# Optimization experiments

Measured on AMD Instinct MI355X. Metric: run time of the kernel, lower is better.

The kernel has to match this reference:

```python
import jax, jax.numpy as jnp
import numpy as np

B, S, D = 2, 2048, 1024
H, DK, DV = 16, 64, 64
NEG = -1e9

def setup_inputs() -> dict:
    key = jax.random.key(0)
    ks = jax.random.split(key, 7)
    scale = 1.0 / np.sqrt(D)
    return {
        "Q": jax.random.normal(ks[0], (B, S, D), dtype=jnp.float32),
        "K": jax.random.normal(ks[1], (B, S, D), dtype=jnp.float32),
        "V": jax.random.normal(ks[2], (B, S, D), dtype=jnp.float32),
        "Wq": jax.random.normal(ks[3], (D, H * DK), dtype=jnp.float32) * scale,
        "Wk": jax.random.normal(ks[4], (D, H * DK), dtype=jnp.float32) * scale,
        "Wv": jax.random.normal(ks[5], (D, H * DV), dtype=jnp.float32) * scale,
        "Wo": jax.random.normal(ks[6], (H * DV, D), dtype=jnp.float32) * scale,
    }

def reference(Q, K, V, Wq, Wk, Wv, Wo):
    b, sq, _ = Q.shape
    sk = K.shape[1]
    # project and split heads: [b, h, s, d]
    q = (Q @ Wq).reshape(b, sq, H, DK).transpose(0, 2, 1, 3)
    k = (K @ Wk).reshape(b, sk, H, DK).transpose(0, 2, 1, 3)
    v = (V @ Wv).reshape(b, sk, H, DV).transpose(0, 2, 1, 3)
    scores = jnp.einsum("bhqd,bhkd->bhqk", q, k) / jnp.sqrt(jnp.float32(DK))
    causal = jnp.tril(jnp.ones((sq, sk), dtype=bool))
    scores = jnp.where(causal[None, None], scores, NEG)
    attn = jax.nn.softmax(scores, axis=-1)
    out = jnp.einsum("bhqk,bhkd->bhqd", attn, v)
    out = out.transpose(0, 2, 1, 3).reshape(b, sq, H * DV)
    return out @ Wo
```

## Files before the change

kernel.cpp:

```cpp
#include <hip/hip_runtime.h>
#include <cstdint>
#include <cstddef>


typedef __bf16 bf16x8 __attribute__((ext_vector_type(8)));
typedef __bf16 bf16x4 __attribute__((ext_vector_type(4)));
typedef float f32x4 __attribute__((ext_vector_type(4)));
typedef unsigned int u32x4 __attribute__((ext_vector_type(4)));

#define MFMA __builtin_amdgcn_mfma_f32_16x16x32_bf16

static __device__ __forceinline__ __bf16 f2b(float f) { return (__bf16)f; }

static __device__ __forceinline__ void gload_lds16(const void* g, void* l) {
  __builtin_amdgcn_global_load_lds(
      (const __attribute__((address_space(1))) void*)g,
      (__attribute__((address_space(3))) void*)l, 16, 0, 0);
}

__global__ __launch_bounds__(256) void wtrans_kernel(
    const float* __restrict__ w0, const float* __restrict__ w1,
    const float* __restrict__ w2, const float* __restrict__ w3,
    __bf16* __restrict__ outT)
{
  const int z = blockIdx.z;
  const float* W = (z == 0) ? w0 : (z == 1) ? w1 : (z == 2) ? w2 : w3;
  __bf16* O = outT + (size_t)z * 1048576;
  __shared__ float t[32][33];
  const int tx = threadIdx.x & 31, ty = threadIdx.x >> 5;
  const int kb = blockIdx.y * 32, nb = blockIdx.x * 32;
#pragma unroll
  for (int i = 0; i < 4; i++)
    t[ty + i * 8][tx] = W[(size_t)(kb + ty + i * 8) * 1024 + nb + tx];
  __syncthreads();
#pragma unroll
  for (int i = 0; i < 4; i++)
    O[(size_t)(nb + ty + i * 8) * 1024 + kb + tx] = f2b(t[tx][ty + i * 8]);
}

__global__ __launch_bounds__(256) void cvt_kernel(
    const float* __restrict__ a0, const float* __restrict__ a1,
    const float* __restrict__ a2, __bf16* __restrict__ o0,
    __bf16* __restrict__ o1, __bf16* __restrict__ o2)
{
  const int z = blockIdx.y;
  const float* src = (z == 0) ? a0 : (z == 1) ? a1 : a2;
  __bf16* dst = (z == 0) ? o0 : (z == 1) ? o1 : o2;
  const int idx = blockIdx.x * 256 + threadIdx.x;
#pragma unroll
  for (int it = 0; it < 4; ++it) {
    const size_t c = (size_t)(idx + it * 131072) * 8;
    f32x4 v0 = *(const f32x4*)&src[c];
    f32x4 v1 = *(const f32x4*)&src[c + 4];
    bf16x8 w = {f2b(v0[0]), f2b(v0[1]), f2b(v0[2]), f2b(v0[3]),
                f2b(v1[0]), f2b(v1[1]), f2b(v1[2]), f2b(v1[3])};
    *(bf16x8*)&dst[c] = w;
  }
}

__global__ __launch_bounds__(256) void gemm_proj_bf16_kernel(
    const __bf16* __restrict__ A0, const __bf16* __restrict__ A1,
    const __bf16* __restrict__ A2, const __bf16* __restrict__ WT,
    __bf16* __restrict__ C0, __bf16* __restrict__ C1, __bf16* __restrict__ C2)
{
  const int z = blockIdx.y;
  const __bf16* A = (z == 0) ? A0 : (z == 1) ? A1 : A2;
  const __bf16* W = WT + (size_t)z * 1048576;
  __bf16* C = (z == 0) ? C0 : (z == 1) ? C1 : C2;

  const int bid = blockIdx.x;
  const int t = (bid & 7) * 32 + (bid >> 3);
  const int mt = t >> 3, nt = t & 7;
  const int mbase = mt * 128, nbase = nt * 128;

  __shared__ __align__(16) __bf16 As[128][32];
  __shared__ __align__(16) __bf16 Bs[128][32];

  const int tid = threadIdx.x;
  const int wid = tid >> 6, lane = tid & 63;
  const int wr = wid >> 1, wc = wid & 1;
  const int lr = lane & 15, kg = lane >> 4;

  f32x4 acc[4][4] = {};

  const int srow = tid >> 2, scol = (tid & 3) * 8;
  const int wbase = tid & 192;

  for (int kb = 0; kb < 32; ++kb) {
    const int k0 = kb * 32;
    __syncthreads();
#pragma unroll
    for (int p = 0; p < 2; ++p) {
      const int r = srow + p * 64;
      gload_lds16(&A[(size_t)(mbase + r) * 1024 + k0 + scol],
                  (__bf16*)As + (size_t)(p * 256 + wbase) * 8);
      gload_lds16(&W[(size_t)(nbase + r) * 1024 + k0 + scol],
                  (__bf16*)Bs + (size_t)(p * 256 + wbase) * 8);
    }
    __syncthreads();

    bf16x8 af[4], bfr[4];
#pragma unroll
    for (int i = 0; i < 4; i++) af[i] = *(const bf16x8*)&As[wr * 64 + i * 16 + lr][kg * 8];
#pragma unroll
    for (int j = 0; j < 4; j++) bfr[j] = *(const bf16x8*)&Bs[wc * 64 + j * 16 + lr][kg * 8];
#pragma unroll
    for (int i = 0; i < 4; i++)
#pragma unroll
      for (int j = 0; j < 4; j++)
        acc[i][j] = MFMA(af[i], bfr[j], acc[i][j], 0, 0, 0);
  }

  if (z == 2) {
#pragma unroll
    for (int i = 0; i < 4; i++)
#pragma unroll
      for (int j = 0; j < 4; j++) {
        const int m0 = mbase + wr * 64 + i * 16 + kg * 4;
        const int n = nbase + wc * 64 + j * 16 + lr;
        const int b = m0 >> 11, s = m0 & 2047, h = n >> 6, dv = n & 63;
        bf16x4 w;
#pragma unroll
        for (int r = 0; r < 4; r++) w[r] = f2b(acc[i][j][r]);
        *(bf16x4*)&C[(((size_t)(b * 16 + h)) * 64 + dv) * 2048 + s] = w;
      }
  } else {
#pragma unroll
    for (int i = 0; i < 4; i++)
#pragma unroll
      for (int j = 0; j < 4; j++)
#pragma unroll
        for (int r = 0; r < 4; r++) {
          const int m = mbase + wr * 64 + i * 16 + kg * 4 + r;
          const int n = nbase + wc * 64 + j * 16 + lr;
          const int b = m >> 11, s = m & 2047, h = n >> 6, dk = n & 63;
          C[(((size_t)(b * 16 + h)) * 2048 + s) * 64 + dk] = f2b(acc[i][j][r]);
        }
  }
}

__global__ __launch_bounds__(256) void gemm_proj_f32_kernel(
    const float* __restrict__ A0, const float* __restrict__ A1,
    const float* __restrict__ A2, const __bf16* __restrict__ WT,
    __bf16* __restrict__ C0, __bf16* __restrict__ C1, __bf16* __restrict__ C2)
{
  const int z = blockIdx.y;
  const float* A = (z == 0) ? A0 : (z == 1) ? A1 : A2;
  const __bf16* W = WT + (size_t)z * 1048576;
  __bf16* C = (z == 0) ? C0 : (z == 1) ? C1 : C2;

  const int mt = blockIdx.x >> 3, nt = blockIdx.x & 7;
  const int mbase = mt * 128, nbase = nt * 128;

  __shared__ __align__(16) __bf16 As[128][40];
  __shared__ __align__(16) __bf16 Bs[128][40];

  const int tid = threadIdx.x;
  const int wid = tid >> 6, lane = tid & 63;
  const int wr = wid >> 1, wc = wid & 1;
  const int lr = lane & 15, kg = lane >> 4;

  f32x4 acc[4][4] = {};
  const int arow = tid >> 3, ac0 = (tid & 7) * 4;

  for (int kb = 0; kb < 32; ++kb) {
    const int k0 = kb * 32;
#pragma unroll
    for (int p = 0; p < 4; ++p) {
      const int r = arow + p * 32;
      f32x4 av = *(const f32x4*)&A[(size_t)(mbase + r) * 1024 + k0 + ac0];
      bf16x4 cv = {f2b(av[0]), f2b(av[1]), f2b(av[2]), f2b(av[3])};
      *(bf16x4*)&As[r][ac0] = cv;
    }
#pragma unroll
    for (int p = 0; p < 2; ++p) {
      const int idx = p * 256 + tid;
      const int r = idx >> 2, c8 = (idx & 3) * 8;
      *(u32x4*)&Bs[r][c8] = *(const u32x4*)&W[(size_t)(nbase + r) * 1024 + k0 + c8];
    }
    __syncthreads();

    bf16x8 af[4], bfr[4];
#pragma unroll
    for (int i = 0; i < 4; i++) af[i] = *(const bf16x8*)&As[wr * 64 + i * 16 + lr][kg * 8];
#pragma unroll
    for (int j = 0; j < 4; j++) bfr[j] = *(const bf16x8*)&Bs[wc * 64 + j * 16 + lr][kg * 8];
#pragma unroll
    for (int i = 0; i < 4; i++)
#pragma unroll
      for (int j = 0; j < 4; j++)
        acc[i][j] = MFMA(af[i], bfr[j], acc[i][j], 0, 0, 0);
    __syncthreads();
  }

  if (z == 2) {
#pragma unroll
    for (int i = 0; i < 4; i++)
#pragma unroll
      for (int j = 0; j < 4; j++) {
        const int m0 = mbase + wr * 64 + i * 16 + kg * 4;
        const int n = nbase + wc * 64 + j * 16 + lr;
        const int b = m0 >> 11, s = m0 & 2047, h = n >> 6, dv = n & 63;
        bf16x4 w;
#pragma unroll
        for (int r = 0; r < 4; r++) w[r] = f2b(acc[i][j][r]);
        *(bf16x4*)&C[(((size_t)(b * 16 + h)) * 64 + dv) * 2048 + s] = w;
      }
  } else {
#pragma unroll
    for (int i = 0; i < 4; i++)
#pragma unroll
      for (int j = 0; j < 4; j++)
#pragma unroll
        for (int r = 0; r < 4; r++) {
          const int m = mbase + wr * 64 + i * 16 + kg * 4 + r;
          const int n = nbase + wc * 64 + j * 16 + lr;
          const int b = m >> 11, s = m & 2047, h = n >> 6, dk = n & 63;
          C[(((size_t)(b * 16 + h)) * 2048 + s) * 64 + dk] = f2b(acc[i][j][r]);
        }
  }
}

__global__ __launch_bounds__(256) void attn_kernel(
    const __bf16* __restrict__ Qh, const __bf16* __restrict__ Kh,
    const __bf16* __restrict__ VTh, __bf16* __restrict__ AO)
{
  const int lin = blockIdx.y * 16 + blockIdx.x;
  const int l = (lin & 7) * 64 + (lin >> 3);
  const int xp = l & 15, bh = l >> 4;
  const int b = bh >> 4, h = bh & 15;
  const __bf16* Qp = Qh + (size_t)bh * 2048 * 64;
  const __bf16* Kp = Kh + (size_t)bh * 2048 * 64;
  const __bf16* Vp = VTh + (size_t)bh * 64 * 2048;

  __shared__ __align__(16) __bf16 Ks[2][64][72];
  __shared__ __align__(16) __bf16 Vt[2][64][72];
  __shared__ __align__(16) __bf16 Ps[4][16][72];

  const int tid = threadIdx.x, wid = tid >> 6, lane = tid & 63;
  const int lr = lane & 15, kg = lane >> 4;
  const int sr0 = tid >> 3, sc0 = (tid & 7) * 8;
  const float SCALE = 0.125f * 1.44269504f;

#pragma unroll
  for (int phase = 0; phase < 2; ++phase) {
    const int qblk = phase ? (31 - xp) : xp;
    const int qbase = qblk << 6;
    const int nkv = qblk + 1;
    const int wq = qbase + wid * 16;

    bf16x8 qf0 = *(const bf16x8*)&Qp[(size_t)(wq + lr) * 64 + kg * 8];
    bf16x8 qf1 = *(const bf16x8*)&Qp[(size_t)(wq + lr) * 64 + 32 + kg * 8];

    f32x4 ot[4] = {};
    float mrow = -1e30f, lsum = 0.f;

    u32x4 kr0 = *(const u32x4*)&Kp[(size_t)sr0 * 64 + sc0];
    u32x4 kr1 = *(const u32x4*)&Kp[(size_t)(sr0 + 32) * 64 + sc0];
    u32x4 vr0 = *(const u32x4*)&Vp[(size_t)sr0 * 2048 + sc0];
    u32x4 vr1 = *(const u32x4*)&Vp[(size_t)(sr0 + 32) * 2048 + sc0];
    __syncthreads();
    *(u32x4*)&Ks[0][sr0][sc0] = kr0;
    *(u32x4*)&Ks[0][sr0 + 32][sc0] = kr1;
    *(u32x4*)&Vt[0][sr0][sc0] = vr0;
    *(u32x4*)&Vt[0][sr0 + 32][sc0] = vr1;

    int cur = 0;
    for (int t = 0; t < nkv; ++t) {
      const int kv0 = t << 6;
      const bool pre = (t + 1 < nkv);
      if (pre) {
        const int nkv0 = kv0 + 64;
        kr0 = *(const u32x4*)&Kp[(size_t)(nkv0 + sr0) * 64 + sc0];
        kr1 = *(const u32x4*)&Kp[(size_t)(nkv0 + sr0 + 32) * 64 + sc0];
        vr0 = *(const u32x4*)&Vp[(size_t)sr0 * 2048 + nkv0 + sc0];
        vr1 = *(const u32x4*)&Vp[(size_t)(sr0 + 32) * 2048 + nkv0 + sc0];
      }
      __syncthreads();

      if (kv0 <= wq + 15) {
        f32x4 st[4] = {};
        __builtin_amdgcn_s_setprio(1);
#pragma unroll
        for (int kvt = 0; kvt < 4; ++kvt) {
          bf16x8 kf0 = *(const bf16x8*)&Ks[cur][kvt * 16 + lr][kg * 8];
          bf16x8 kf1 = *(const bf16x8*)&Ks[cur][kvt * 16 + lr][32 + kg * 8];
          st[kvt] = MFMA(kf0, qf0, st[kvt], 0, 0, 0);
          st[kvt] = MFMA(kf1, qf1, st[kvt], 0, 0, 0);
        }
        __builtin_amdgcn_s_setprio(0);

        const int qidx = wq + lr;
        const bool needmask = (kv0 + 63) > wq;
        float sv[16];
        float mx = -1e30f;
#pragma unroll
        for (int kvt = 0; kvt < 4; ++kvt)
#pragma unroll
          for (int r = 0; r < 4; ++r) {
            float v = st[kvt][r] * SCALE;
            if (needmask && (kv0 + kvt * 16 + kg * 4 + r > qidx)) v = -1e30f;
            sv[kvt * 4 + r] = v;
            mx = fmaxf(mx, v);
          }
        mx = fmaxf(mx, __shfl_xor(mx, 16));
        mx = fmaxf(mx, __shfl_xor(mx, 32));
        const float mnew = fmaxf(mrow, mx);
        const float scl = exp2f(mrow - mnew);
        mrow = mnew;
        float rs = 0.f;
#pragma unroll
        for (int kvt = 0; kvt < 4; ++kvt) {
          bf16x4 pk;
#pragma unroll
          for (int r = 0; r < 4; ++r) {
            const float p = exp2f(sv[kvt * 4 + r] - mnew);
            rs += p;
            pk[r] = f2b(p);
          }
          *(bf16x4*)&Ps[wid][lr][kvt * 16 + kg * 4] = pk;
        }
        rs += __shfl_xor(rs, 16);
        rs += __shfl_xor(rs, 32);
        lsum = lsum * scl + rs;
#pragma unroll
        for (int dvt = 0; dvt < 4; ++dvt) ot[dvt] *= scl;

#pragma unroll
        for (int h2 = 0; h2 < 2; ++h2) {
          bf16x8 pf = *(const bf16x8*)&Ps[wid][lr][h2 * 32 + kg * 8];
          __builtin_amdgcn_s_setprio(1);
#pragma unroll
          for (int dvt = 0; dvt < 4; ++dvt) {
            bf16x8 vf = *(const bf16x8*)&Vt[cur][dvt * 16 + lr][h2 * 32 + kg * 8];
            ot[dvt] = MFMA(vf, pf, ot[dvt], 0, 0, 0);
          }
          __builtin_amdgcn_s_setprio(0);
        }
      }

      if (pre) {
        const int nb = cur ^ 1;
        *(u32x4*)&Ks[nb][sr0][sc0] = kr0;
        *(u32x4*)&Ks[nb][sr0 + 32][sc0] = kr1;
        *(u32x4*)&Vt[nb][sr0][sc0] = vr0;
        *(u32x4*)&Vt[nb][sr0 + 32][sc0] = vr1;
      }
      cur ^= 1;
    }

    const float rl = 1.f / lsum;
    const int q = wq + lr;
#pragma unroll
    for (int dvt = 0; dvt < 4; ++dvt) {
      bf16x4 w;
#pragma unroll
      for (int r = 0; r < 4; ++r) w[r] = f2b(ot[dvt][r] * rl);
      *(bf16x4*)&AO[((size_t)(b * 2048 + q)) * 1024 + h * 64 + dvt * 16 + kg * 4] = w;
    }
  }
}

__global__ __launch_bounds__(256) void gemm_out_kernel(
    const __bf16* __restrict__ A, const __bf16* __restrict__ WT,
    float* __restrict__ Out)
{
  const int bid = blockIdx.x;
  const int t = (bid & 7) * 32 + (bid >> 3);
  const int mt = t >> 3, nt = t & 7;
  const int mbase = mt * 128, nbase = nt * 128;

  __shared__ __align__(16) __bf16 As[128][32];
  __shared__ __align__(16) __bf16 Bs[128][32];

  const int tid = threadIdx.x;
  const int wid = tid >> 6, lane = tid & 63;
  const int wr = wid >> 1, wc = wid & 1;
  const int lr = lane & 15, kg = lane >> 4;

  f32x4 acc[4][4] = {};

  const int srow = tid >> 2, scol = (tid & 3) * 8;
  const int wbase = tid & 192;

  for (int kb = 0; kb < 32; ++kb) {
    const int k0 = kb * 32;
    __syncthreads();
#pragma unroll
    for (int p = 0; p < 2; ++p) {
      const int r = srow + p * 64;
      gload_lds16(&A[(size_t)(mbase + r) * 1024 + k0 + scol],
                  (__bf16*)As + (size_t)(p * 256 + wbase) * 8);
      gload_lds16(&WT[(size_t)(nbase + r) * 1024 + k0 + scol],
                  (__bf16*)Bs + (size_t)(p * 256 + wbase) * 8);
    }
    __syncthreads();

    bf16x8 af[4], bfr[4];
#pragma unroll
    for (int i = 0; i < 4; i++) af[i] = *(const bf16x8*)&As[wr * 64 + i * 16 + lr][kg * 8];
#pragma unroll
    for (int j = 0; j < 4; j++) bfr[j] = *(const bf16x8*)&Bs[wc * 64 + j * 16 + lr][kg * 8];
#pragma unroll
    for (int i = 0; i < 4; i++)
#pragma unroll
      for (int j = 0; j < 4; j++)
        acc[i][j] = MFMA(af[i], bfr[j], acc[i][j], 0, 0, 0);
  }

#pragma unroll
  for (int i = 0; i < 4; i++)
#pragma unroll
    for (int j = 0; j < 4; j++)
#pragma unroll
      for (int r = 0; r < 4; r++) {
        const int m = mbase + wr * 64 + i * 16 + kg * 4 + r;
        const int n = nbase + wc * 64 + j * 16 + lr;
        Out[(size_t)m * 1024 + n] = acc[i][j][r];
      }
}

extern "C" void kernel_launch(void* const* d_in, const int* in_sizes, int n_in,
                              void* d_out, int out_size, void* d_ws, size_t ws_size,
                              hipStream_t stream) {
  const float* Q  = (const float*)d_in[0];
  const float* K  = (const float*)d_in[1];
  const float* V  = (const float*)d_in[2];
  const float* Wq = (const float*)d_in[3];
  const float* Wk = (const float*)d_in[4];
  const float* Wv = (const float*)d_in[5];
  const float* Wo = (const float*)d_in[6];
  float* out = (float*)d_out;

  const size_t M4 = 4194304;
  __bf16* wT  = (__bf16*)d_ws;
  __bf16* qb  = wT + M4;
  __bf16* kb  = qb + M4;
  __bf16* vtb = kb + M4;

  const bool fast = ws_size >= (size_t)(28 * 1048576) * 2;

  wtrans_kernel<<<dim3(32, 32, 4), 256, 0, stream>>>(Wq, Wk, Wv, Wo, wT);

  __bf16* ao;
  if (fast) {
    __bf16* qa = vtb + M4;
    __bf16* ka = qa + M4;
    __bf16* va = ka + M4;
    ao = qa;
    cvt_kernel<<<dim3(512, 3), 256, 0, stream>>>(Q, K, V, qa, ka, va);
    gemm_proj_bf16_kernel<<<dim3(256, 3), 256, 0, stream>>>(qa, ka, va, wT,
                                                            qb, kb, vtb);
  } else {
    ao = vtb + M4;
    gemm_proj_f32_kernel<<<dim3(256, 3), 256, 0, stream>>>(Q, K, V, wT,
                                                           qb, kb, vtb);
  }

  attn_kernel<<<dim3(16, 32), 256, 0, stream>>>(qb, kb, vtb, ao);
  gemm_out_kernel<<<dim3(256), 256, 0, stream>>>(ao, wT + 3 * 1048576, out);
}
```

Baseline: 137.8 us.

## Fold softmax scale into Q projection, lazy rescale, one q-block per workgroup

After: 138.2 us. No clear change (+0.3%).

```diff
diff --git a/kernel.cpp b/kernel.cpp
--- a/kernel.cpp
+++ b/kernel.cpp
@@ -17,6 +17,8 @@
       (const __attribute__((address_space(1))) void*)g,
       (__attribute__((address_space(3))) void*)l, 16, 0, 0);
 }
+
+#define QSCALE 0.18033688f
 
 __global__ __launch_bounds__(256) void wtrans_kernel(
     const float* __restrict__ w0, const float* __restrict__ w1,
@@ -67,6 +69,7 @@
   const __bf16* A = (z == 0) ? A0 : (z == 1) ? A1 : A2;
   const __bf16* W = WT + (size_t)z * 1048576;
   __bf16* C = (z == 0) ? C0 : (z == 1) ? C1 : C2;
+  const float osc = (z == 0) ? QSCALE : 1.0f;
 
   const int bid = blockIdx.x;
   const int t = (bid & 7) * 32 + (bid >> 3);
@@ -134,7 +137,7 @@
           const int m = mbase + wr * 64 + i * 16 + kg * 4 + r;
           const int n = nbase + wc * 64 + j * 16 + lr;
           const int b = m >> 11, s = m & 2047, h = n >> 6, dk = n & 63;
-          C[(((size_t)(b * 16 + h)) * 2048 + s) * 64 + dk] = f2b(acc[i][j][r]);
+          C[(((size_t)(b * 16 + h)) * 2048 + s) * 64 + dk] = f2b(acc[i][j][r] * osc);
         }
   }
 }
@@ -148,6 +151,7 @@
   const float* A = (z == 0) ? A0 : (z == 1) ? A1 : A2;
   const __bf16* W = WT + (size_t)z * 1048576;
   __bf16* C = (z == 0) ? C0 : (z == 1) ? C1 : C2;
+  const float osc = (z == 0) ? QSCALE : 1.0f;
 
   const int mt = blockIdx.x >> 3, nt = blockIdx.x & 7;
   const int mbase = mt * 128, nbase = nt * 128;
@@ -216,7 +220,7 @@
           const int m = mbase + wr * 64 + i * 16 + kg * 4 + r;
           const int n = nbase + wc * 64 + j * 16 + lr;
           const int b = m >> 11, s = m & 2047, h = n >> 6, dk = n & 63;
-          C[(((size_t)(b * 16 + h)) * 2048 + s) * 64 + dk] = f2b(acc[i][j][r]);
+          C[(((size_t)(b * 16 + h)) * 2048 + s) * 64 + dk] = f2b(acc[i][j][r] * osc);
         }
   }
 }
@@ -225,9 +229,10 @@
     const __bf16* __restrict__ Qh, const __bf16* __restrict__ Kh,
     const __bf16* __restrict__ VTh, __bf16* __restrict__ AO)
 {
-  const int lin = blockIdx.y * 16 + blockIdx.x;
-  const int l = (lin & 7) * 64 + (lin >> 3);
-  const int xp = l & 15, bh = l >> 4;
+  const int lin = blockIdx.x;
+  const int l = (lin & 7) * 128 + (lin >> 3);
+  const int bh = l >> 5;
+  const int qblk = 31 - (l & 31);
   const int b = bh >> 4, h = bh & 15;
   const __bf16* Qp = Qh + (size_t)bh * 2048 * 64;
   const __bf16* Kp = Kh + (size_t)bh * 2048 * 64;
@@ -240,124 +245,125 @@
   const int tid = threadIdx.x, wid = tid >> 6, lane = tid & 63;
   const int lr = lane & 15, kg = lane >> 4;
   const int sr0 = tid >> 3, sc0 = (tid & 7) * 8;
-  const float SCALE = 0.125f * 1.44269504f;
-
-#pragma unroll
-  for (int phase = 0; phase < 2; ++phase) {
-    const int qblk = phase ? (31 - xp) : xp;
-    const int qbase = qblk << 6;
-    const int nkv = qblk + 1;
-    const int wq = qbase + wid * 16;
-
-    bf16x8 qf0 = *(const bf16x8*)&Qp[(size_t)(wq + lr) * 64 + kg * 8];
-    bf16x8 qf1 = *(const bf16x8*)&Qp[(size_t)(wq + lr) * 64 + 32 + kg * 8];
-
-    f32x4 ot[4] = {};
-    float mrow = -1e30f, lsum = 0.f;
-
-    u32x4 kr0 = *(const u32x4*)&Kp[(size_t)sr0 * 64 + sc0];
-    u32x4 kr1 = *(const u32x4*)&Kp[(size_t)(sr0 + 32) * 64 + sc0];
-    u32x4 vr0 = *(const u32x4*)&Vp[(size_t)sr0 * 2048 + sc0];
-    u32x4 vr1 = *(const u32x4*)&Vp[(size_t)(sr0 + 32) * 2048 + sc0];
-    __syncthreads();
-    *(u32x4*)&Ks[0][sr0][sc0] = kr0;
-    *(u32x4*)&Ks[0][sr0 + 32][sc0] = kr1;
-    *(u32x4*)&Vt[0][sr0][sc0] = vr0;
-    *(u32x4*)&Vt[0][sr0 + 32][sc0] = vr1;
-
-    int cur = 0;
-    for (int t = 0; t < nkv; ++t) {
-      const int kv0 = t << 6;
-      const bool pre = (t + 1 < nkv);
-      if (pre) {
-        const int nkv0 = kv0 + 64;
-        kr0 = *(const u32x4*)&Kp[(size_t)(nkv0 + sr0) * 64 + sc0];
-        kr1 = *(const u32x4*)&Kp[(size_t)(nkv0 + sr0 + 32) * 64 + sc0];
-        vr0 = *(const u32x4*)&Vp[(size_t)sr0 * 2048 + nkv0 + sc0];
-        vr1 = *(const u32x4*)&Vp[(size_t)(sr0 + 32) * 2048 + nkv0 + sc0];
+
+  const int qbase = qblk << 6;
+  const int nkv = qblk + 1;
+  const int wq = qbase + wid * 16;
+
+  bf16x8 qf0 = *(const bf16x8*)&Qp[(size_t)(wq + lr) * 64 + kg * 8];
+  bf16x8 qf1 = *(const bf16x8*)&Qp[(size_t)(wq + lr) * 64 + 32 + kg * 8];
+
+  f32x4 ot[4] = {};
+  float mrow = -1e30f, lsum = 0.f;
+
+  u32x4 kr0 = *(const u32x4*)&Kp[(size_t)sr0 * 64 + sc0];
+  u32x4 kr1 = *(const u32x4*)&Kp[(size_t)(sr0 + 32) * 64 + sc0];
+  u32x4 vr0 = *(const u32x4*)&Vp[(size_t)sr0 * 2048 + sc0];
+  u32x4 vr1 = *(const u32x4*)&Vp[(size_t)(sr0 + 32) * 2048 + sc0];
+  *(u32x4*)&Ks[0][sr0][sc0] = kr0;
+  *(u32x4*)&Ks[0][sr0 + 32][sc0] = kr1;
+  *(u32x4*)&Vt[0][sr0][sc0] = vr0;
+  *(u32x4*)&Vt[0][sr0 + 32][sc0] = vr1;
+
+  int cur = 0;
+  for (int t = 0; t < nkv; ++t) {
+    const bool pre = (t + 1 < nkv);
+    if (pre) {
+      const int n0 = (t + 1) << 6;
+      kr0 = *(const u32x4*)&Kp[(size_t)(n0 + sr0) * 64 + sc0];
+      kr1 = *(const u32x4*)&Kp[(size_t)(n0 + sr0 + 32) * 64 + sc0];
+      vr0 = *(const u32x4*)&Vp[(size_t)sr0 * 2048 + n0 + sc0];
+      vr1 = *(const u32x4*)&Vp[(size_t)(sr0 + 32) * 2048 + n0 + sc0];
+    }
+    __syncthreads();
+
+    f32x4 st[4] = {};
+    __builtin_amdgcn_s_setprio(1);
+#pragma unroll
+    for (int kvt = 0; kvt < 4; ++kvt) {
+      bf16x8 kf0 = *(const bf16x8*)&Ks[cur][kvt * 16 + lr][kg * 8];
+      bf16x8 kf1 = *(const bf16x8*)&Ks[cur][kvt * 16 + lr][32 + kg * 8];
+      st[kvt] = MFMA(kf0, qf0, st[kvt], 0, 0, 0);
+      st[kvt] = MFMA(kf1, qf1, st[kvt], 0, 0, 0);
+    }
+    __builtin_amdgcn_s_setprio(0);
+
+    float sv[16];
+#pragma unroll
+    for (int kvt = 0; kvt < 4; ++kvt)
+#pragma unroll
+      for (int r = 0; r < 4; ++r) sv[kvt * 4 + r] = st[kvt][r];
+    if (t == nkv - 1) {
+      const int qidx = wq + lr;
+      const int kvb = t << 6;
+#pragma unroll
+      for (int kvt = 0; kvt < 4; ++kvt)
+#pragma unroll
+        for (int r = 0; r < 4; ++r)
+          if (kvb + kvt * 16 + kg * 4 + r > qidx) sv[kvt * 4 + r] = -1e30f;
+    }
+    float mx = fmaxf(fmaxf(sv[0], sv[1]), sv[2]);
+    mx = fmaxf(fmaxf(mx, sv[3]), sv[4]);
+    mx = fmaxf(fmaxf(mx, sv[5]), sv[6]);
+    mx = fmaxf(fmaxf(mx, sv[7]), sv[8]);
+    mx = fmaxf(fmaxf(mx, sv[9]), sv[10]);
+    mx = fmaxf(fmaxf(mx, sv[11]), sv[12]);
+    mx = fmaxf(fmaxf(mx, sv[13]), sv[14]);
+    mx = fmaxf(mx, sv[15]);
+    mx = fmaxf(mx, __shfl_xor(mx, 16));
+    mx = fmaxf(mx, __shfl_xor(mx, 32));
+    if (__any(mx > mrow + 8.f)) {
+      const float mnew = fmaxf(mrow, mx);
+      const float scl = exp2f(mrow - mnew);
+      mrow = mnew;
+      lsum *= scl;
+#pragma unroll
+      for (int dvt = 0; dvt < 4; ++dvt) ot[dvt] *= scl;
+    }
+#pragma unroll
+    for (int kvt = 0; kvt < 4; ++kvt) {
+      bf16x4 pk;
+#pragma unroll
+      for (int r = 0; r < 4; ++r) {
+        const float p = exp2f(sv[kvt * 4 + r] - mrow);
+        lsum += p;
+        pk[r] = f2b(p);
       }
-      __syncthreads();
-
-      if (kv0 <= wq + 15) {
-        f32x4 st[4] = {};
-        __builtin_amdgcn_s_setprio(1);
-#pragma unroll
-        for (int kvt = 0; kvt < 4; ++kvt) {
-          bf16x8 kf0 = *(const bf16x8*)&Ks[cur][kvt * 16 + lr][kg * 8];
-          bf16x8 kf1 = *(const bf16x8*)&Ks[cur][kvt * 16 + lr][32 + kg * 8];
-          st[kvt] = MFMA(kf0, qf0, st[kvt], 0, 0, 0);
-          st[kvt] = MFMA(kf1, qf1, st[kvt], 0, 0, 0);
-        }
-        __builtin_amdgcn_s_setprio(0);
-
-        const int qidx = wq + lr;
-        const bool needmask = (kv0 + 63) > wq;
-        float sv[16];
-        float mx = -1e30f;
-#pragma unroll
-        for (int kvt = 0; kvt < 4; ++kvt)
-#pragma unroll
-          for (int r = 0; r < 4; ++r) {
-            float v = st[kvt][r] * SCALE;
-            if (needmask && (kv0 + kvt * 16 + kg * 4 + r > qidx)) v = -1e30f;
-            sv[kvt * 4 + r] = v;
-            mx = fmaxf(mx, v);
-          }
-        mx = fmaxf(mx, __shfl_xor(mx, 16));
-        mx = fmaxf(mx, __shfl_xor(mx, 32));
-        const float mnew = fmaxf(mrow, mx);
-        const float scl = exp2f(mrow - mnew);
-        mrow = mnew;
-        float rs = 0.f;
-#pragma unroll
-        for (int kvt = 0; kvt < 4; ++kvt) {
-          bf16x4 pk;
-#pragma unroll
-          for (int r = 0; r < 4; ++r) {
-            const float p = exp2f(sv[kvt * 4 + r] - mnew);
-            rs += p;
-            pk[r] = f2b(p);
-          }
-          *(bf16x4*)&Ps[wid][lr][kvt * 16 + kg * 4] = pk;
-        }
-        rs += __shfl_xor(rs, 16);
-        rs += __shfl_xor(rs, 32);
-        lsum = lsum * scl + rs;
-#pragma unroll
-        for (int dvt = 0; dvt < 4; ++dvt) ot[dvt] *= scl;
-
-#pragma unroll
-        for (int h2 = 0; h2 < 2; ++h2) {
-          bf16x8 pf = *(const bf16x8*)&Ps[wid][lr][h2 * 32 + kg * 8];
-          __builtin_amdgcn_s_setprio(1);
-#pragma unroll
-          for (int dvt = 0; dvt < 4; ++dvt) {
-            bf16x8 vf = *(const bf16x8*)&Vt[cur][dvt * 16 + lr][h2 * 32 + kg * 8];
-            ot[dvt] = MFMA(vf, pf, ot[dvt], 0, 0, 0);
-          }
-          __builtin_amdgcn_s_setprio(0);
-        }
+      *(bf16x4*)&Ps[wid][lr][kvt * 16 + kg * 4] = pk;
+    }
+
+#pragma unroll
+    for (int h2 = 0; h2 < 2; ++h2) {
+      bf16x8 pf = *(const bf16x8*)&Ps[wid][lr][h2 * 32 + kg * 8];
+      __builtin_amdgcn_s_setprio(1);
+#pragma unroll
+      for (int dvt = 0; dvt < 4; ++dvt) {
+        bf16x8 vf = *(const bf16x8*)&Vt[cur][dvt * 16 + lr][h2 * 32 + kg * 8];
+        ot[dvt] = MFMA(vf, pf, ot[dvt], 0, 0, 0);
       }
-
-      if (pre) {
-        const int nb = cur ^ 1;
-        *(u32x4*)&Ks[nb][sr0][sc0] = kr0;
-        *(u32x4*)&Ks[nb][sr0 + 32][sc0] = kr1;
-        *(u32x4*)&Vt[nb][sr0][sc0] = vr0;
-        *(u32x4*)&Vt[nb][sr0 + 32][sc0] = vr1;
-      }
-      cur ^= 1;
-    }
-
-    const float rl = 1.f / lsum;
-    const int q = wq + lr;
-#pragma unroll
-    for (int dvt = 0; dvt < 4; ++dvt) {
-      bf16x4 w;
-#pragma unroll
-      for (int r = 0; r < 4; ++r) w[r] = f2b(ot[dvt][r] * rl);
-      *(bf16x4*)&AO[((size_t)(b * 2048 + q)) * 1024 + h * 64 + dvt * 16 + kg * 4] = w;
-    }
+      __builtin_amdgcn_s_setprio(0);
+    }
+
+    if (pre) {
+      const int nb = cur ^ 1;
+      *(u32x4*)&Ks[nb][sr0][sc0] = kr0;
+      *(u32x4*)&Ks[nb][sr0 + 32][sc0] = kr1;
+      *(u32x4*)&Vt[nb][sr0][sc0] = vr0;
+      *(u32x4*)&Vt[nb][sr0 + 32][sc0] = vr1;
+    }
+    cur ^= 1;
+  }
+
+  lsum += __shfl_xor(lsum, 16);
+  lsum += __shfl_xor(lsum, 32);
+  const float rl = 1.f / lsum;
+  const int q = wq + lr;
+#pragma unroll
+  for (int dvt = 0; dvt < 4; ++dvt) {
+    bf16x4 w;
+#pragma unroll
+    for (int r = 0; r < 4; ++r) w[r] = f2b(ot[dvt][r] * rl);
+    *(bf16x4*)&AO[((size_t)(b * 2048 + q)) * 1024 + h * 64 + dvt * 16 + kg * 4] = w;
   }
 }
 
@@ -457,6 +463,6 @@
                                                            qb, kb, vtb);
   }
 
-  attn_kernel<<<dim3(16, 32), 256, 0, stream>>>(qb, kb, vtb, ao);
+  attn_kernel<<<dim3(1024), 256, 0, stream>>>(qb, kb, vtb, ao);
   gemm_out_kernel<<<dim3(256), 256, 0, stream>>>(ao, wT + 3 * 1048576, out);
 }
```
